# Optimization experiments

Hardware: AMD Instinct MI355X
Metric: run time of the kernel (lower is better)

The kernel has to match this reference:

```python
import jax, jax.numpy as jnp
import numpy as np

N, E = 20000, 320000          # nodes, edges (avg degree 16)
IN, OUT, EC = 256, 256, 64    # in_channels == out_channels (required by BN placement)
BN_EPS = 1e-5


def setup_inputs() -> dict:
    key = jax.random.key(0)
    ks = jax.random.split(key, 8)
    def lin(k, fan_in, fan_out):
        # kaiming-uniform-ish init like nn.Linear
        bound = 1.0 / np.sqrt(fan_in)
        return jax.random.uniform(k, (fan_in, fan_out), jnp.float32, -bound, bound)
    return {
        "x": jax.random.normal(ks[0], (N, IN), jnp.float32),
        "edge_index": jax.random.randint(ks[1], (2, E), 0, N),
        "edge_attr": jax.random.normal(ks[2], (E, EC), jnp.float32),
        "W_edge": lin(ks[3], EC, IN),          # edge_lin (no bias)
        "W_rel": lin(ks[4], IN, OUT),           # GraphConv lin_rel weight
        "b_rel": jnp.zeros((OUT,), jnp.float32),  # GraphConv lin_rel bias
        "W_root": lin(ks[5], IN, OUT),          # GraphConv lin_root (no bias)
        "gamma": jnp.ones((OUT,), jnp.float32),  # BN weight
        "beta": jnp.zeros((OUT,), jnp.float32),  # BN bias
        "W_res": lin(ks[6], IN, OUT),           # res_lin (no bias)
    }


def reference(x, edge_index, edge_attr, W_edge, W_rel, b_rel, W_root, gamma, beta, W_res):
    src, dst = edge_index[0], edge_index[1]
    # edge feature projection: [E, EC] -> [E, IN]
    e = edge_attr @ W_edge
    # message passing: gather source node feats, modulate by edge feats, scatter-add to dst
    msg = x[src] * e                                   # [E, IN]
    agg = jax.ops.segment_sum(msg, dst, num_segments=x.shape[0])  # [N, IN]
    # GraphConv: lin_rel(aggregate) + lin_root(x)
    h = agg @ W_rel + b_rel + x @ W_root               # [N, OUT]
    h = jax.nn.relu(h)
    # BatchNorm1d (training mode: batch statistics over nodes)
    mean = h.mean(axis=0)
    var = ((h - mean) ** 2).mean(axis=0)
    h = (h - mean) * jax.lax.rsqrt(var + BN_EPS) * gamma + beta
    # residual branch
    return h + x @ W_res
```

## Files before the change

### kernel.cpp

```cpp
#include <hip/hip_runtime.h>
#include <hip/hip_bf16.h>


#define N_NODES 20000
#define E_EDGES 320000
#define C 256
#define CE 64
#define MAXDEG 64
#define BN_EPS 1e-5f

typedef __attribute__((ext_vector_type(8))) short short8;
typedef __attribute__((ext_vector_type(8))) unsigned short ushort8;
typedef __attribute__((ext_vector_type(4))) float f32x4;
typedef __attribute__((ext_vector_type(4))) unsigned short ushort4v;

static __device__ __forceinline__ float bf2f(unsigned short u) {
    union { unsigned int i; float f; } v; v.i = (unsigned int)u << 16; return v.f;
}
static __device__ __forceinline__ unsigned short f2bf(float f) {
    __hip_bfloat16 h = __float2bfloat16(f);
    return *reinterpret_cast<unsigned short*>(&h);
}

__global__ __launch_bounds__(256) void k_wprep(
    const float* __restrict__ W_rel, const float* __restrict__ W_root,
    const float* __restrict__ W_res, const float* __restrict__ W_edge,
    unsigned short* __restrict__ wt_hi, unsigned short* __restrict__ wt_lo,
    unsigned short* __restrict__ wte_hi, unsigned short* __restrict__ wte_lo) {
    int b = blockIdx.x, n = threadIdx.x;
    if (b < 768) {
        int m = b >> 8, k = b & 255;
        const float* W = (m == 0) ? W_rel : (m == 1) ? W_root : W_res;
        float w = W[k * C + n];
        unsigned short h = f2bf(w), l = f2bf(w - bf2f(h));
        size_t o = (((size_t)m * 16 + (n >> 4)) * 8 + (k >> 5)) * 512
                 + (size_t)(((n & 15) | (((k >> 3) & 3) << 4)) * 8) + (k & 7);
        wt_hi[o] = h; wt_lo[o] = l;
    } else {
        int k = b - 768;
        float w = W_edge[k * C + n];
        unsigned short h = f2bf(w), l = f2bf(w - bf2f(h));
        size_t o = ((size_t)(n >> 4) * 2 + (k >> 5)) * 512
                 + (size_t)(((n & 15) | (((k >> 3) & 3) << 4)) * 8) + (k & 7);
        wte_hi[o] = h; wte_lo[o] = l;
    }
}

__global__ void k_bucket(const int* __restrict__ ei, int* __restrict__ deg,
                         int2* __restrict__ elist2) {
    int e = blockIdx.x * blockDim.x + threadIdx.x;
    if (e < E_EDGES) {
        int d = ei[E_EDGES + e];
        int s = ei[e];
        int slot = atomicAdd(&deg[d], 1);
        if (slot < MAXDEG) elist2[d * MAXDEG + slot] = make_int2(e, s);
    }
}

__global__ __launch_bounds__(256, 2) void k_edgemm(
    const float* __restrict__ ea, const unsigned short* __restrict__ wte_hi,
    const unsigned short* __restrict__ wte_lo,
    unsigned short* __restrict__ e_mat) {
    __shared__ short lds[16384];
    short* a_hi = lds;
    short* a_lo = lds + 4096;
    const int tid = threadIdx.x;
    const int e0 = blockIdx.x * 64;

#pragma unroll
    for (int i = 0; i < 4; ++i) {
        int f = tid + 256 * i;
        int r = f >> 4, k4 = (f & 15) * 4;
        float4 v = *reinterpret_cast<const float4*>(&ea[(size_t)(e0 + r) * CE + k4]);
        unsigned short h0 = f2bf(v.x), h1 = f2bf(v.y), h2 = f2bf(v.z), h3 = f2bf(v.w);
        ushort4v hv = {h0, h1, h2, h3};
        ushort4v lv = {f2bf(v.x - bf2f(h0)), f2bf(v.y - bf2f(h1)),
                       f2bf(v.z - bf2f(h2)), f2bf(v.w - bf2f(h3))};
        int byte = (r * CE + k4) * 2;
        int swz = byte ^ ((r & 7) << 4);
        *reinterpret_cast<ushort4v*>((char*)a_hi + swz) = hv;
        *reinterpret_cast<ushort4v*>((char*)a_lo + swz) = lv;
    }
    __syncthreads();

    const int w = tid >> 6, l = tid & 63;
    const int c0 = w * 64;
    f32x4 acc[4][4];
#pragma unroll
    for (int rt = 0; rt < 4; ++rt)
#pragma unroll
        for (int ct = 0; ct < 4; ++ct) acc[rt][ct] = (f32x4){0.f, 0.f, 0.f, 0.f};

#pragma unroll
    for (int ks = 0; ks < 2; ++ks) {
        short8 ah[4], al[4];
#pragma unroll
        for (int rt = 0; rt < 4; ++rt) {
            int r = rt * 16 + (l & 15);
            int byte = (r * CE + ks * 32 + (l >> 4) * 8) * 2;
            int swz = byte ^ ((r & 7) << 4);
            ah[rt] = *reinterpret_cast<const short8*>((const char*)a_hi + swz);
            al[rt] = *reinterpret_cast<const short8*>((const char*)a_lo + swz);
        }
#pragma unroll
        for (int ct = 0; ct < 4; ++ct) {
            int nt = (c0 >> 4) + ct;
            size_t off = ((size_t)nt * 2 + ks) * 512 + (size_t)l * 8;
            short8 bh = *reinterpret_cast<const short8*>(&wte_hi[off]);
            short8 bl = *reinterpret_cast<const short8*>(&wte_lo[off]);
#pragma unroll
            for (int rt = 0; rt < 4; ++rt) {
                acc[rt][ct] = __builtin_amdgcn_mfma_f32_16x16x32_bf16(ah[rt], bh, acc[rt][ct], 0, 0, 0);
                acc[rt][ct] = __builtin_amdgcn_mfma_f32_16x16x32_bf16(al[rt], bh, acc[rt][ct], 0, 0, 0);
                acc[rt][ct] = __builtin_amdgcn_mfma_f32_16x16x32_bf16(ah[rt], bl, acc[rt][ct], 0, 0, 0);
            }
        }
    }

    __syncthreads();
#pragma unroll
    for (int rt = 0; rt < 4; ++rt)
#pragma unroll
        for (int ct = 0; ct < 4; ++ct) {
            int col = c0 + ct * 16 + (l & 15);
#pragma unroll
            for (int q = 0; q < 4; ++q) {
                int r = rt * 16 + (l >> 4) * 4 + q;
                lds[r * C + col] = (short)f2bf(acc[rt][ct][q]);
            }
        }
    __syncthreads();
#pragma unroll
    for (int i = 0; i < 8; ++i) {
        int f = tid + 256 * i;
        int r = f >> 5, c8 = (f & 31) * 8;
        *reinterpret_cast<ushort8*>(&e_mat[(size_t)(e0 + r) * C + c8]) =
            *reinterpret_cast<const ushort8*>(&lds[r * C + c8]);
    }
}

__global__ __launch_bounds__(128) void k_aggregate(
    const float* __restrict__ x, const unsigned short* __restrict__ e_mat,
    const int* __restrict__ deg, const int2* __restrict__ elist2,
    float* __restrict__ agg) {
    const int c2 = threadIdx.x;
    const int lane = threadIdx.x & 63;
    for (int node = blockIdx.x; node < N_NODES; node += gridDim.x) {
        int dr = deg[node];
        int d = __builtin_amdgcn_readfirstlane(dr < MAXDEG ? dr : MAXDEG);
        float accx = 0.f, accy = 0.f;
        if (d > 0) {
            int2 pr = elist2[node * MAXDEG + (lane < d ? lane : 0)];
            for (int i = 0; i < d; i += 4) {
                int m = d - i;
                unsigned int ev[4]; float2 xv[4];
#pragma unroll
                for (int j = 0; j < 4; ++j) {
                    if (j < m) {
                        int e = __shfl(pr.x, i + j);
                        int s = __shfl(pr.y, i + j);
                        ev[j] = *reinterpret_cast<const unsigned int*>(
                                    &e_mat[(size_t)e * C + c2 * 2]);
                        xv[j] = *reinterpret_cast<const float2*>(
                                    &x[(size_t)s * C + c2 * 2]);
                    } else { ev[j] = 0; xv[j] = make_float2(0.f, 0.f); }
                }
#pragma unroll
                for (int j = 0; j < 4; ++j) {
                    accx += bf2f((unsigned short)(ev[j] & 0xffff)) * xv[j].x;
                    accy += bf2f((unsigned short)(ev[j] >> 16)) * xv[j].y;
                }
            }
        }
        *reinterpret_cast<float2*>(&agg[(size_t)node * C + c2 * 2]) =
            make_float2(accx, accy);
    }
}

__global__ __launch_bounds__(256, 2) void k_gemm(
    const float* aggt_r, const float* __restrict__ x,
    const unsigned short* __restrict__ wt_hi,
    const unsigned short* __restrict__ wt_lo,
    const float* __restrict__ b_rel, float* t, float* __restrict__ out,
    float* __restrict__ chsum, float* __restrict__ chsumsq) {
    __shared__ short ah_[32 * C], al_[32 * C];
    __shared__ short xh_[32 * C], xl_[32 * C];
    const int tid = threadIdx.x;
    const int n0 = blockIdx.x * 32;

#pragma unroll
    for (int i = 0; i < 8; ++i) {
        int f = tid + 256 * i;
        int r = f >> 6, k4 = (f & 63) * 4;
        float4 av = *reinterpret_cast<const float4*>(&aggt_r[(size_t)(n0 + r) * C + k4]);
        float4 xv = *reinterpret_cast<const float4*>(&x[(size_t)(n0 + r) * C + k4]);
        int byte = (r * C + k4) * 2;
        int swz = byte ^ ((r & 7) << 4);
        unsigned short h0 = f2bf(av.x), h1 = f2bf(av.y), h2 = f2bf(av.z), h3 = f2bf(av.w);
        ushort4v hv = {h0, h1, h2, h3};
        ushort4v lv = {f2bf(av.x - bf2f(h0)), f2bf(av.y - bf2f(h1)),
                       f2bf(av.z - bf2f(h2)), f2bf(av.w - bf2f(h3))};
        *reinterpret_cast<ushort4v*>((char*)ah_ + swz) = hv;
        *reinterpret_cast<ushort4v*>((char*)al_ + swz) = lv;
        h0 = f2bf(xv.x); h1 = f2bf(xv.y); h2 = f2bf(xv.z); h3 = f2bf(xv.w);
        ushort4v hx = {h0, h1, h2, h3};
        ushort4v lx = {f2bf(xv.x - bf2f(h0)), f2bf(xv.y - bf2f(h1)),
                       f2bf(xv.z - bf2f(h2)), f2bf(xv.w - bf2f(h3))};
        *reinterpret_cast<ushort4v*>((char*)xh_ + swz) = hx;
        *reinterpret_cast<ushort4v*>((char*)xl_ + swz) = lx;
    }
    __syncthreads();

    const int w = tid >> 6, l = tid & 63;
    const int c0 = w * 64;
    f32x4 acc[2][3][4];
#pragma unroll
    for (int rt = 0; rt < 2; ++rt)
#pragma unroll
        for (int mat = 0; mat < 3; ++mat)
#pragma unroll
            for (int ct = 0; ct < 4; ++ct) acc[rt][mat][ct] = (f32x4){0.f, 0.f, 0.f, 0.f};

#pragma unroll 1
    for (int ks = 0; ks < 8; ++ks) {
        short8 fa[2][4];
#pragma unroll
        for (int rt = 0; rt < 2; ++rt) {
            int r = rt * 16 + (l & 15);
            int byte = (r * C + ks * 32 + (l >> 4) * 8) * 2;
            int swz = byte ^ ((r & 7) << 4);
            fa[rt][0] = *reinterpret_cast<const short8*>((const char*)ah_ + swz);
            fa[rt][1] = *reinterpret_cast<const short8*>((const char*)al_ + swz);
            fa[rt][2] = *reinterpret_cast<const short8*>((const char*)xh_ + swz);
            fa[rt][3] = *reinterpret_cast<const short8*>((const char*)xl_ + swz);
        }
#pragma unroll
        for (int mat = 0; mat < 3; ++mat) {
            const int hi = (mat == 0) ? 0 : 2, lo = hi + 1;
#pragma unroll
            for (int ct = 0; ct < 4; ++ct) {
                int nt = (c0 >> 4) + ct;
                size_t off = (((size_t)mat * 16 + nt) * 8 + ks) * 512 + (size_t)l * 8;
                short8 bh = *reinterpret_cast<const short8*>(&wt_hi[off]);
                short8 bl = *reinterpret_cast<const short8*>(&wt_lo[off]);
#pragma unroll
                for (int rt = 0; rt < 2; ++rt) {
                    acc[rt][mat][ct] = __builtin_amdgcn_mfma_f32_16x16x32_bf16(fa[rt][hi], bh, acc[rt][mat][ct], 0, 0, 0);
                    acc[rt][mat][ct] = __builtin_amdgcn_mfma_f32_16x16x32_bf16(fa[rt][lo], bh, acc[rt][mat][ct], 0, 0, 0);
                    acc[rt][mat][ct] = __builtin_amdgcn_mfma_f32_16x16x32_bf16(fa[rt][hi], bl, acc[rt][mat][ct], 0, 0, 0);
                }
            }
        }
    }

    float s1[4], s2[4];
#pragma unroll
    for (int ct = 0; ct < 4; ++ct) { s1[ct] = 0.f; s2[ct] = 0.f; }
#pragma unroll
    for (int ct = 0; ct < 4; ++ct) {
        int col = c0 + ct * 16 + (l & 15);
        float bias = b_rel[col];
#pragma unroll
        for (int rt = 0; rt < 2; ++rt) {
            f32x4 hrel = acc[rt][0][ct], hroot = acc[rt][1][ct], hres = acc[rt][2][ct];
#pragma unroll
            for (int q = 0; q < 4; ++q) {
                int node = n0 + rt * 16 + (l >> 4) * 4 + q;
                float h = fmaxf(hrel[q] + hroot[q] + bias, 0.f);
                s1[ct] += h; s2[ct] += h * h;
                t[(size_t)node * C + col] = h;
                out[(size_t)node * C + col] = hres[q];
            }
        }
    }
#pragma unroll
    for (int ct = 0; ct < 4; ++ct) {
        s1[ct] += __shfl_xor(s1[ct], 16); s1[ct] += __shfl_xor(s1[ct], 32);
        s2[ct] += __shfl_xor(s2[ct], 16); s2[ct] += __shfl_xor(s2[ct], 32);
    }
    if ((l >> 4) == 0) {
#pragma unroll
        for (int ct = 0; ct < 4; ++ct) {
            int col = c0 + ct * 16 + l;
            atomicAdd(&chsum[col], s1[ct]);
            atomicAdd(&chsumsq[col], s2[ct]);
        }
    }
}

__global__ __launch_bounds__(256) void k_finalize(
    const float* __restrict__ t, const float* __restrict__ chsum,
    const float* __restrict__ chsumsq, const float* __restrict__ gamma,
    const float* __restrict__ beta, float* out) {
    const float invN = 1.f / (float)N_NODES;
    int i = (blockIdx.x * blockDim.x + threadIdx.x) * 4;
    if (i >= N_NODES * C) return;
    int c = i & (C - 1);
    float4 tv = *reinterpret_cast<const float4*>(&t[i]);
    float4 rv = *reinterpret_cast<const float4*>(&out[i]);
    float4 o;
    {
        float m = chsum[c + 0] * invN;
        float v = chsumsq[c + 0] * invN - m * m;
        o.x = (tv.x - m) * rsqrtf(v + BN_EPS) * gamma[c + 0] + beta[c + 0] + rv.x;
    }
    {
        float m = chsum[c + 1] * invN;
        float v = chsumsq[c + 1] * invN - m * m;
        o.y = (tv.y - m) * rsqrtf(v + BN_EPS) * gamma[c + 1] + beta[c + 1] + rv.y;
    }
    {
        float m = chsum[c + 2] * invN;
        float v = chsumsq[c + 2] * invN - m * m;
        o.z = (tv.z - m) * rsqrtf(v + BN_EPS) * gamma[c + 2] + beta[c + 2] + rv.z;
    }
    {
        float m = chsum[c + 3] * invN;
        float v = chsumsq[c + 3] * invN - m * m;
        o.w = (tv.w - m) * rsqrtf(v + BN_EPS) * gamma[c + 3] + beta[c + 3] + rv.w;
    }
    *reinterpret_cast<float4*>(&out[i]) = o;
}

extern "C" void kernel_launch(void* const* d_in, const int* in_sizes, int n_in,
                              void* d_out, int out_size, void* d_ws, size_t ws_size,
                              hipStream_t stream) {
    const float* x      = (const float*)d_in[0];
    const int*   ei     = (const int*)  d_in[1];
    const float* ea     = (const float*)d_in[2];
    const float* W_edge = (const float*)d_in[3];
    const float* W_rel  = (const float*)d_in[4];
    const float* b_rel  = (const float*)d_in[5];
    const float* W_root = (const float*)d_in[6];
    const float* gamma  = (const float*)d_in[7];
    const float* beta   = (const float*)d_in[8];
    const float* W_res  = (const float*)d_in[9];
    float* out = (float*)d_out;

    float* ws      = (float*)d_ws;
    float* aggt    = ws;
    float* chsum   = ws + (size_t)N_NODES * C;
    float* chsumsq = chsum + C;
    int*   deg     = (int*)(chsumsq + C);
    int2*  elist2  = (int2*)(deg + N_NODES);
    unsigned short* e_mat  = (unsigned short*)(elist2 + (size_t)N_NODES * MAXDEG);
    unsigned short* wte_hi = e_mat + (size_t)E_EDGES * C;
    unsigned short* wte_lo = wte_hi + C * CE;
    unsigned short* wt_hi  = wte_lo + C * CE;
    unsigned short* wt_lo  = wt_hi + 3 * C * C;
    size_t need = (char*)(wt_lo + 3 * C * C) - (char*)d_ws;
    if (ws_size < need) return;

    hipMemsetAsync(chsum, 0, 2 * C * sizeof(float) + N_NODES * sizeof(int), stream);

    k_wprep<<<832, 256, 0, stream>>>(W_rel, W_root, W_res, W_edge,
                                     wt_hi, wt_lo, wte_hi, wte_lo);
    k_bucket<<<(E_EDGES + 255) / 256, 256, 0, stream>>>(ei, deg, elist2);
    k_edgemm<<<E_EDGES / 64, 256, 0, stream>>>(ea, wte_hi, wte_lo, e_mat);
    k_aggregate<<<10000, 128, 0, stream>>>(x, e_mat, deg, elist2, aggt);
    k_gemm<<<N_NODES / 32, 256, 0, stream>>>(aggt, x, wt_hi, wt_lo, b_rel,
                                             aggt, out, chsum, chsumsq);
    k_finalize<<<(N_NODES * C / 4 + 255) / 256, 256, 0, stream>>>(
        aggt, chsum, chsumsq, gamma, beta, out);
}
```

Measured before the change: 378.4 us.

## Drop weight low-part MFMAs, split GEMM per matrix, move BN stats to separate kernel

Weights are now converted only to a single bf16 part, so the split-precision product drops from three MFMAs to two (activation hi/lo times weight hi). The fused three-matrix GEMM is split into a grid dimension per weight matrix with smaller LDS use and higher occupancy bounds. LDS tiles are stored in MFMA fragment order instead of XOR-swizzled rows. ReLU and BN statistics move into a new k_bnstat kernel, and the finalize kernel now reads the two raw GEMM outputs and recomputes ReLU. This adds extra global traffic for two N×C fp32 intermediates and lowers weight precision.

After: 335.9 us. 1.13x faster.

```diff
diff --git a/kernel.cpp b/kernel.cpp
--- a/kernel.cpp
+++ b/kernel.cpp
@@ -25,24 +25,19 @@
 __global__ __launch_bounds__(256) void k_wprep(
     const float* __restrict__ W_rel, const float* __restrict__ W_root,
     const float* __restrict__ W_res, const float* __restrict__ W_edge,
-    unsigned short* __restrict__ wt_hi, unsigned short* __restrict__ wt_lo,
-    unsigned short* __restrict__ wte_hi, unsigned short* __restrict__ wte_lo) {
+    unsigned short* __restrict__ wt_hi, unsigned short* __restrict__ wte_hi) {
     int b = blockIdx.x, n = threadIdx.x;
     if (b < 768) {
         int m = b >> 8, k = b & 255;
         const float* W = (m == 0) ? W_rel : (m == 1) ? W_root : W_res;
-        float w = W[k * C + n];
-        unsigned short h = f2bf(w), l = f2bf(w - bf2f(h));
         size_t o = (((size_t)m * 16 + (n >> 4)) * 8 + (k >> 5)) * 512
                  + (size_t)(((n & 15) | (((k >> 3) & 3) << 4)) * 8) + (k & 7);
-        wt_hi[o] = h; wt_lo[o] = l;
+        wt_hi[o] = f2bf(W[k * C + n]);
     } else {
         int k = b - 768;
-        float w = W_edge[k * C + n];
-        unsigned short h = f2bf(w), l = f2bf(w - bf2f(h));
         size_t o = ((size_t)(n >> 4) * 2 + (k >> 5)) * 512
                  + (size_t)(((n & 15) | (((k >> 3) & 3) << 4)) * 8) + (k & 7);
-        wte_hi[o] = h; wte_lo[o] = l;
+        wte_hi[o] = f2bf(W_edge[k * C + n]);
     }
 }
 
@@ -57,13 +52,10 @@
     }
 }
 
-__global__ __launch_bounds__(256, 2) void k_edgemm(
+__global__ __launch_bounds__(256, 3) void k_edgemm(
     const float* __restrict__ ea, const unsigned short* __restrict__ wte_hi,
-    const unsigned short* __restrict__ wte_lo,
     unsigned short* __restrict__ e_mat) {
     __shared__ short lds[16384];
-    short* a_hi = lds;
-    short* a_lo = lds + 4096;
     const int tid = threadIdx.x;
     const int e0 = blockIdx.x * 64;
 
@@ -76,15 +68,15 @@
         ushort4v hv = {h0, h1, h2, h3};
         ushort4v lv = {f2bf(v.x - bf2f(h0)), f2bf(v.y - bf2f(h1)),
                        f2bf(v.z - bf2f(h2)), f2bf(v.w - bf2f(h3))};
-        int byte = (r * CE + k4) * 2;
-        int swz = byte ^ ((r & 7) << 4);
-        *reinterpret_cast<ushort4v*>((char*)a_hi + swz) = hv;
-        *reinterpret_cast<ushort4v*>((char*)a_lo + swz) = lv;
+        int rt = r >> 4, ks = k4 >> 5;
+        int lane = (r & 15) | (((k4 >> 3) & 3) << 4);
+        int base = (((rt * 2 + ks) * 2 + 0) * 64 + lane) * 8 + (k4 & 7);
+        *reinterpret_cast<ushort4v*>(&lds[base]) = hv;
+        *reinterpret_cast<ushort4v*>(&lds[base + 512]) = lv;
     }
     __syncthreads();
 
     const int w = tid >> 6, l = tid & 63;
-    const int c0 = w * 64;
     f32x4 acc[4][4];
 #pragma unroll
     for (int rt = 0; rt < 4; ++rt)
@@ -93,36 +85,34 @@
 
 #pragma unroll
     for (int ks = 0; ks < 2; ++ks) {
+        short8 b[4];
+#pragma unroll
+        for (int ct = 0; ct < 4; ++ct) {
+            int nt = w * 4 + ct;
+            b[ct] = *reinterpret_cast<const short8*>(&wte_hi[(size_t)(nt * 2 + ks) * 512 + l * 8]);
+        }
         short8 ah[4], al[4];
 #pragma unroll
         for (int rt = 0; rt < 4; ++rt) {
-            int r = rt * 16 + (l & 15);
-            int byte = (r * CE + ks * 32 + (l >> 4) * 8) * 2;
-            int swz = byte ^ ((r & 7) << 4);
-            ah[rt] = *reinterpret_cast<const short8*>((const char*)a_hi + swz);
-            al[rt] = *reinterpret_cast<const short8*>((const char*)a_lo + swz);
-        }
+            int base = ((rt * 2 + ks) * 2) * 512 + l * 8;
+            ah[rt] = *reinterpret_cast<const short8*>(&lds[base]);
+            al[rt] = *reinterpret_cast<const short8*>(&lds[base + 512]);
+        }
+#pragma unroll
+        for (int ct = 0; ct < 4; ++ct)
+#pragma unroll
+            for (int rt = 0; rt < 4; ++rt) {
+                acc[rt][ct] = __builtin_amdgcn_mfma_f32_16x16x32_bf16(ah[rt], b[ct], acc[rt][ct], 0, 0, 0);
+                acc[rt][ct] = __builtin_amdgcn_mfma_f32_16x16x32_bf16(al[rt], b[ct], acc[rt][ct], 0, 0, 0);
+            }
+    }
+
+    __syncthreads();
+#pragma unroll
+    for (int rt = 0; rt < 4; ++rt)
 #pragma unroll
         for (int ct = 0; ct < 4; ++ct) {
-            int nt = (c0 >> 4) + ct;
-            size_t off = ((size_t)nt * 2 + ks) * 512 + (size_t)l * 8;
-            short8 bh = *reinterpret_cast<const short8*>(&wte_hi[off]);
-            short8 bl = *reinterpret_cast<const short8*>(&wte_lo[off]);
-#pragma unroll
-            for (int rt = 0; rt < 4; ++rt) {
-                acc[rt][ct] = __builtin_amdgcn_mfma_f32_16x16x32_bf16(ah[rt], bh, acc[rt][ct], 0, 0, 0);
-                acc[rt][ct] = __builtin_amdgcn_mfma_f32_16x16x32_bf16(al[rt], bh, acc[rt][ct], 0, 0, 0);
-                acc[rt][ct] = __builtin_amdgcn_mfma_f32_16x16x32_bf16(ah[rt], bl, acc[rt][ct], 0, 0, 0);
-            }
-        }
-    }
-
-    __syncthreads();
-#pragma unroll
-    for (int rt = 0; rt < 4; ++rt)
-#pragma unroll
-        for (int ct = 0; ct < 4; ++ct) {
-            int col = c0 + ct * 16 + (l & 15);
+            int col = w * 64 + ct * 16 + (l & 15);
 #pragma unroll
             for (int q = 0; q < 4; ++q) {
                 int r = rt * 16 + (l >> 4) * 4 + q;
@@ -177,147 +167,157 @@
     }
 }
 
-__global__ __launch_bounds__(256, 2) void k_gemm(
-    const float* aggt_r, const float* __restrict__ x,
+__global__ __launch_bounds__(256, 4) void k_gemm(
+    const float* __restrict__ aggt, const float* __restrict__ x,
     const unsigned short* __restrict__ wt_hi,
-    const unsigned short* __restrict__ wt_lo,
-    const float* __restrict__ b_rel, float* t, float* __restrict__ out,
-    float* __restrict__ chsum, float* __restrict__ chsumsq) {
-    __shared__ short ah_[32 * C], al_[32 * C];
-    __shared__ short xh_[32 * C], xl_[32 * C];
+    float* __restrict__ g_rel, float* __restrict__ g_root,
+    float* __restrict__ g_res) {
+    __shared__ short AB[16384];
     const int tid = threadIdx.x;
     const int n0 = blockIdx.x * 32;
+    const int mat = blockIdx.y;
+    const float* Asrc = (mat == 0) ? aggt : x;
+    float* dst = (mat == 0) ? g_rel : (mat == 1) ? g_root : g_res;
 
 #pragma unroll
     for (int i = 0; i < 8; ++i) {
         int f = tid + 256 * i;
         int r = f >> 6, k4 = (f & 63) * 4;
-        float4 av = *reinterpret_cast<const float4*>(&aggt_r[(size_t)(n0 + r) * C + k4]);
-        float4 xv = *reinterpret_cast<const float4*>(&x[(size_t)(n0 + r) * C + k4]);
-        int byte = (r * C + k4) * 2;
-        int swz = byte ^ ((r & 7) << 4);
-        unsigned short h0 = f2bf(av.x), h1 = f2bf(av.y), h2 = f2bf(av.z), h3 = f2bf(av.w);
+        float4 v = *reinterpret_cast<const float4*>(&Asrc[(size_t)(n0 + r) * C + k4]);
+        unsigned short h0 = f2bf(v.x), h1 = f2bf(v.y), h2 = f2bf(v.z), h3 = f2bf(v.w);
         ushort4v hv = {h0, h1, h2, h3};
-        ushort4v lv = {f2bf(av.x - bf2f(h0)), f2bf(av.y - bf2f(h1)),
-                       f2bf(av.z - bf2f(h2)), f2bf(av.w - bf2f(h3))};
-        *reinterpret_cast<ushort4v*>((char*)ah_ + swz) = hv;
-        *reinterpret_cast<ushort4v*>((char*)al_ + swz) = lv;
-        h0 = f2bf(xv.x); h1 = f2bf(xv.y); h2 = f2bf(xv.z); h3 = f2bf(xv.w);
-        ushort4v hx = {h0, h1, h2, h3};
-        ushort4v lx = {f2bf(xv.x - bf2f(h0)), f2bf(xv.y - bf2f(h1)),
-                       f2bf(xv.z - bf2f(h2)), f2bf(xv.w - bf2f(h3))};
-        *reinterpret_cast<ushort4v*>((char*)xh_ + swz) = hx;
-        *reinterpret_cast<ushort4v*>((char*)xl_ + swz) = lx;
+        ushort4v lv = {f2bf(v.x - bf2f(h0)), f2bf(v.y - bf2f(h1)),
+                       f2bf(v.z - bf2f(h2)), f2bf(v.w - bf2f(h3))};
+        int rt = r >> 4, ks = k4 >> 5;
+        int lane = (r & 15) | (((k4 >> 3) & 3) << 4);
+        int base = (((rt * 8 + ks) * 2 + 0) * 64 + lane) * 8 + (k4 & 7);
+        *reinterpret_cast<ushort4v*>(&AB[base]) = hv;
+        *reinterpret_cast<ushort4v*>(&AB[base + 512]) = lv;
     }
     __syncthreads();
 
     const int w = tid >> 6, l = tid & 63;
-    const int c0 = w * 64;
-    f32x4 acc[2][3][4];
+    f32x4 acc[2][4];
 #pragma unroll
     for (int rt = 0; rt < 2; ++rt)
 #pragma unroll
-        for (int mat = 0; mat < 3; ++mat)
-#pragma unroll
-            for (int ct = 0; ct < 4; ++ct) acc[rt][mat][ct] = (f32x4){0.f, 0.f, 0.f, 0.f};
-
-#pragma unroll 1
+        for (int ct = 0; ct < 4; ++ct) acc[rt][ct] = (f32x4){0.f, 0.f, 0.f, 0.f};
+
+    const unsigned short* wbase = wt_hi + (size_t)mat * 16 * 8 * 512;
+
+#pragma unroll
     for (int ks = 0; ks < 8; ++ks) {
-        short8 fa[2][4];
+        short8 b[4];
+#pragma unroll
+        for (int ct = 0; ct < 4; ++ct) {
+            int nt = w * 4 + ct;
+            b[ct] = *reinterpret_cast<const short8*>(&wbase[(size_t)(nt * 8 + ks) * 512 + l * 8]);
+        }
+        short8 ah[2], al[2];
 #pragma unroll
         for (int rt = 0; rt < 2; ++rt) {
-            int r = rt * 16 + (l & 15);
-            int byte = (r * C + ks * 32 + (l >> 4) * 8) * 2;
-            int swz = byte ^ ((r & 7) << 4);
-            fa[rt][0] = *reinterpret_cast<const short8*>((const char*)ah_ + swz);
-            fa[rt][1] = *reinterpret_cast<const short8*>((const char*)al_ + swz);
-            fa[rt][2] = *reinterpret_cast<const short8*>((const char*)xh_ + swz);
-            fa[rt][3] = *reinterpret_cast<const short8*>((const char*)xl_ + swz);
-        }
-#pragma unroll
-        for (int mat = 0; mat < 3; ++mat) {
-            const int hi = (mat == 0) ? 0 : 2, lo = hi + 1;
-#pragma unroll
-            for (int ct = 0; ct < 4; ++ct) {
-                int nt = (c0 >> 4) + ct;
-                size_t off = (((size_t)mat * 16 + nt) * 8 + ks) * 512 + (size_t)l * 8;
-                short8 bh = *reinterpret_cast<const short8*>(&wt_hi[off]);
-                short8 bl = *reinterpret_cast<const short8*>(&wt_lo[off]);
-#pragma unroll
-                for (int rt = 0; rt < 2; ++rt) {
-                    acc[rt][mat][ct] = __builtin_amdgcn_mfma_f32_16x16x32_bf16(fa[rt][hi], bh, acc[rt][mat][ct], 0, 0, 0);
-                    acc[rt][mat][ct] = __builtin_amdgcn_mfma_f32_16x16x32_bf16(fa[rt][lo], bh, acc[rt][mat][ct], 0, 0, 0);
-                    acc[rt][mat][ct] = __builtin_amdgcn_mfma_f32_16x16x32_bf16(fa[rt][hi], bl, acc[rt][mat][ct], 0, 0, 0);
-                }
-            }
-        }
-    }
-
-    float s1[4], s2[4];
-#pragma unroll
-    for (int ct = 0; ct < 4; ++ct) { s1[ct] = 0.f; s2[ct] = 0.f; }
+            int base = ((rt * 8 + ks) * 2) * 512 + l * 8;
+            ah[rt] = *reinterpret_cast<const short8*>(&AB[base]);
+            al[rt] = *reinterpret_cast<const short8*>(&AB[base + 512]);
+        }
+#pragma unroll
+        for (int ct = 0; ct < 4; ++ct)
+#pragma unroll
+            for (int rt = 0; rt < 2; ++rt) {
+                acc[rt][ct] = __builtin_amdgcn_mfma_f32_16x16x32_bf16(ah[rt], b[ct], acc[rt][ct], 0, 0, 0);
+                acc[rt][ct] = __builtin_amdgcn_mfma_f32_16x16x32_bf16(al[rt], b[ct], acc[rt][ct], 0, 0, 0);
+            }
+    }
+
 #pragma unroll
     for (int ct = 0; ct < 4; ++ct) {
-        int col = c0 + ct * 16 + (l & 15);
-        float bias = b_rel[col];
-#pragma unroll
-        for (int rt = 0; rt < 2; ++rt) {
-            f32x4 hrel = acc[rt][0][ct], hroot = acc[rt][1][ct], hres = acc[rt][2][ct];
+        int col = w * 64 + ct * 16 + (l & 15);
+#pragma unroll
+        for (int rt = 0; rt < 2; ++rt)
 #pragma unroll
             for (int q = 0; q < 4; ++q) {
                 int node = n0 + rt * 16 + (l >> 4) * 4 + q;
-                float h = fmaxf(hrel[q] + hroot[q] + bias, 0.f);
-                s1[ct] += h; s2[ct] += h * h;
-                t[(size_t)node * C + col] = h;
-                out[(size_t)node * C + col] = hres[q];
-            }
-        }
-    }
-#pragma unroll
-    for (int ct = 0; ct < 4; ++ct) {
-        s1[ct] += __shfl_xor(s1[ct], 16); s1[ct] += __shfl_xor(s1[ct], 32);
-        s2[ct] += __shfl_xor(s2[ct], 16); s2[ct] += __shfl_xor(s2[ct], 32);
-    }
-    if ((l >> 4) == 0) {
-#pragma unroll
-        for (int ct = 0; ct < 4; ++ct) {
-            int col = c0 + ct * 16 + l;
-            atomicAdd(&chsum[col], s1[ct]);
-            atomicAdd(&chsumsq[col], s2[ct]);
-        }
-    }
+                dst[(size_t)node * C + col] = acc[rt][ct][q];
+            }
+    }
+}
+
+__global__ __launch_bounds__(256) void k_bnstat(
+    const float* __restrict__ g_rel, const float* __restrict__ g_root,
+    const float* __restrict__ b_rel, float* __restrict__ chsum,
+    float* __restrict__ chsumsq) {
+    __shared__ float2 red[4 * 256];
+    const int tid = threadIdx.x;
+    const int c0 = (tid & 63) * 4, rg = tid >> 6;
+    const int base = blockIdx.x * 32;
+    float4 b4 = *reinterpret_cast<const float4*>(&b_rel[c0]);
+    float4 s1 = {0.f, 0.f, 0.f, 0.f}, s2 = {0.f, 0.f, 0.f, 0.f};
+#pragma unroll
+    for (int i = 0; i < 8; ++i) {
+        size_t row = (size_t)(base + rg * 8 + i) * C + c0;
+        float4 hr = *reinterpret_cast<const float4*>(&g_rel[row]);
+        float4 ho = *reinterpret_cast<const float4*>(&g_root[row]);
+        float4 h;
+        h.x = fmaxf(hr.x + ho.x + b4.x, 0.f);
+        h.y = fmaxf(hr.y + ho.y + b4.y, 0.f);
+        h.z = fmaxf(hr.z + ho.z + b4.z, 0.f);
+        h.w = fmaxf(hr.w + ho.w + b4.w, 0.f);
+        s1.x += h.x; s1.y += h.y; s1.z += h.z; s1.w += h.w;
+        s2.x += h.x * h.x; s2.y += h.y * h.y;
+        s2.z += h.z * h.z; s2.w += h.w * h.w;
+    }
+    red[rg * 256 + c0 + 0] = make_float2(s1.x, s2.x);
+    red[rg * 256 + c0 + 1] = make_float2(s1.y, s2.y);
+    red[rg * 256 + c0 + 2] = make_float2(s1.z, s2.z);
+    red[rg * 256 + c0 + 3] = make_float2(s1.w, s2.w);
+    __syncthreads();
+    float a = 0.f, bsum = 0.f;
+#pragma unroll
+    for (int g = 0; g < 4; ++g) {
+        float2 v = red[g * 256 + tid];
+        a += v.x; bsum += v.y;
+    }
+    atomicAdd(&chsum[tid], a);
+    atomicAdd(&chsumsq[tid], bsum);
 }
 
 __global__ __launch_bounds__(256) void k_finalize(
-    const float* __restrict__ t, const float* __restrict__ chsum,
+    const float* __restrict__ g_rel, const float* __restrict__ g_root,
+    const float* __restrict__ b_rel, const float* __restrict__ chsum,
     const float* __restrict__ chsumsq, const float* __restrict__ gamma,
     const float* __restrict__ beta, float* out) {
     const float invN = 1.f / (float)N_NODES;
     int i = (blockIdx.x * blockDim.x + threadIdx.x) * 4;
     if (i >= N_NODES * C) return;
     int c = i & (C - 1);
-    float4 tv = *reinterpret_cast<const float4*>(&t[i]);
+    float4 hr = *reinterpret_cast<const float4*>(&g_rel[i]);
+    float4 ho = *reinterpret_cast<const float4*>(&g_root[i]);
+    float4 b4 = *reinterpret_cast<const float4*>(&b_rel[c]);
     float4 rv = *reinterpret_cast<const float4*>(&out[i]);
     float4 o;
     {
+        float h = fmaxf(hr.x + ho.x + b4.x, 0.f);
         float m = chsum[c + 0] * invN;
         float v = chsumsq[c + 0] * invN - m * m;
-        o.x = (tv.x - m) * rsqrtf(v + BN_EPS) * gamma[c + 0] + beta[c + 0] + rv.x;
+        o.x = (h - m) * rsqrtf(v + BN_EPS) * gamma[c + 0] + beta[c + 0] + rv.x;
     }
     {
+        float h = fmaxf(hr.y + ho.y + b4.y, 0.f);
         float m = chsum[c + 1] * invN;
         float v = chsumsq[c + 1] * invN - m * m;
-        o.y = (tv.y - m) * rsqrtf(v + BN_EPS) * gamma[c + 1] + beta[c + 1] + rv.y;
+        o.y = (h - m) * rsqrtf(v + BN_EPS) * gamma[c + 1] + beta[c + 1] + rv.y;
     }
     {
+        float h = fmaxf(hr.z + ho.z + b4.z, 0.f);
         float m = chsum[c + 2] * invN;
         float v = chsumsq[c + 2] * invN - m * m;
-        o.z = (tv.z - m) * rsqrtf(v + BN_EPS) * gamma[c + 2] + beta[c + 2] + rv.z;
+        o.z = (h - m) * rsqrtf(v + BN_EPS) * gamma[c + 2] + beta[c + 2] + rv.z;
     }
     {
+        float h = fmaxf(hr.w + ho.w + b4.w, 0.f);
         float m = chsum[c + 3] * invN;
         float v = chsumsq[c + 3] * invN - m * m;
-        o.w = (tv.w - m) * rsqrtf(v + BN_EPS) * gamma[c + 3] + beta[c + 3] + rv.w;
+        o.w = (h - m) * rsqrtf(v + BN_EPS) * gamma[c + 3] + beta[c + 3] + rv.w;
     }
     *reinterpret_cast<float4*>(&out[i]) = o;
 }
@@ -345,21 +345,21 @@
     int2*  elist2  = (int2*)(deg + N_NODES);
     unsigned short* e_mat  = (unsigned short*)(elist2 + (size_t)N_NODES * MAXDEG);
     unsigned short* wte_hi = e_mat + (size_t)E_EDGES * C;
-    unsigned short* wte_lo = wte_hi + C * CE;
-    unsigned short* wt_hi  = wte_lo + C * CE;
-    unsigned short* wt_lo  = wt_hi + 3 * C * C;
-    size_t need = (char*)(wt_lo + 3 * C * C) - (char*)d_ws;
+    unsigned short* wt_hi  = wte_hi + C * CE;
+    float* g_rel  = (float*)e_mat;
+    float* g_root = g_rel + (size_t)N_NODES * C;
+    size_t need = (char*)(wt_hi + 3 * C * C) - (char*)d_ws;
     if (ws_size < need) return;
 
     hipMemsetAsync(chsum, 0, 2 * C * sizeof(float) + N_NODES * sizeof(int), stream);
 
-    k_wprep<<<832, 256, 0, stream>>>(W_rel, W_root, W_res, W_edge,
-                                     wt_hi, wt_lo, wte_hi, wte_lo);
+    k_wprep<<<832, 256, 0, stream>>>(W_rel, W_root, W_res, W_edge, wt_hi, wte_hi);
     k_bucket<<<(E_EDGES + 255) / 256, 256, 0, stream>>>(ei, deg, elist2);
-    k_edgemm<<<E_EDGES / 64, 256, 0, stream>>>(ea, wte_hi, wte_lo, e_mat);
+    k_edgemm<<<E_EDGES / 64, 256, 0, stream>>>(ea, wte_hi, e_mat);
     k_aggregate<<<10000, 128, 0, stream>>>(x, e_mat, deg, elist2, aggt);
-    k_gemm<<<N_NODES / 32, 256, 0, stream>>>(aggt, x, wt_hi, wt_lo, b_rel,
-                                             aggt, out, chsum, chsumsq);
+    k_gemm<<<dim3(N_NODES / 32, 3), 256, 0, stream>>>(aggt, x, wt_hi,
+                                                      g_rel, g_root, out);
+    k_bnstat<<<N_NODES / 32, 256, 0, stream>>>(g_rel, g_root, b_rel, chsum, chsumsq);
     k_finalize<<<(N_NODES * C / 4 + 255) / 256, 256, 0, stream>>>(
-        aggt, chsum, chsumsq, gamma, beta, out);
-}
+        g_rel, g_root, b_rel, chsum, chsumsq, gamma, beta, out);
+}
```
